# Kernel tuning notes

Hardware: AMD Instinct MI355X
Metric: run time of the kernel (lower is better)

Reference implementation:

```python
import jax, jax.numpy as jnp
import numpy as np

N = 150000   # total supergraph nodes (entities+events+chains)
D = 128      # embed_size
H = 4        # attention heads
DH = D // H  # head dim
E = 300000   # edges per layer
L = 4        # layer_specs length
A = 8        # edge attr dim
T = 10       # num_edge_type
TIME_SCALE = 24.0
SLOPE = 0.2  # negative_slope


def setup_inputs() -> dict:
    key = jax.random.key(0)
    ks = jax.random.split(key, 16)
    nrm = lambda k, s, sc=1.0: jax.random.normal(k, s, dtype=jnp.float32) * sc
    return {
        'x': nrm(ks[0], (N, D), 0.1),
        'Wq': nrm(ks[1], (L, D, D), D ** -0.5),
        'Wk': nrm(ks[2], (L, D, D), D ** -0.5),
        'Wv': nrm(ks[3], (L, D, D), D ** -0.5),
        'Wskip': nrm(ks[4], (L, D, D), D ** -0.5),
        'Wa': nrm(ks[5], (L, A, D), 0.1),
        'time_w': nrm(ks[6], (D,)),
        'time_b': nrm(ks[7], (D,), 0.1),
        'dist_w': nrm(ks[8], (D,)),
        'dist_b': nrm(ks[9], (D,), 0.1),
        'type_table': nrm(ks[10], (T, D), 0.1),
        'bn_gamma': jnp.ones((L, D), jnp.float32),
        'bn_beta': jnp.zeros((L, D), jnp.float32),
        'beta': jnp.full((L,), 0.5, jnp.float32),
        'edge_attr': jax.random.uniform(ks[11], (L, E, A), dtype=jnp.float32),
        'edge_dt': jax.random.uniform(ks[12], (L, E), dtype=jnp.float32) * TIME_SCALE,
        'edge_ds': jax.random.uniform(ks[13], (L, E), dtype=jnp.float32) * 10.0,
        'edge_index': jax.random.randint(ks[14], (L, 2, E), 0, N),
        'edge_type': jax.random.randint(ks[15], (L, E), 0, T),
    }


def _layer(x, Wq, Wk, Wv, Wskip, Wa, time_w, time_b, dist_w, dist_b,
           type_table, gamma, bvec, beta, attr, dt, ds, ei, et):
    n = x.shape[0]
    src, dst = ei[0], ei[1]
    # continuous time / distance encoders: cos basis (TimeEncoder / 'time' DistanceEncoder)
    te = jnp.cos((dt / TIME_SCALE)[:, None] * time_w + time_b)   # [E,D]
    de = jnp.cos(ds[:, None] * dist_w + dist_b)                  # [E,D]
    # 'add' edge/time fusion: attr MLP + time + dist + edge-type embeddings
    edge_feat = attr @ Wa + te + de + type_table[et]             # [E,D]
    kv_in = x[src] + edge_feat                                   # gather + fuse
    q = (x @ Wq).reshape(n, H, DH)[dst]                          # [E,H,DH]
    k = (kv_in @ Wk).reshape(-1, H, DH)
    v = (kv_in @ Wv).reshape(-1, H, DH)
    logits = (q * k).sum(-1) * (DH ** -0.5)                      # [E,H]
    logits = jnp.where(logits >= 0, logits, SLOPE * logits)      # leaky_relu(negative_slope)
    # segment softmax over incoming edges of each destination node
    m = jax.ops.segment_max(logits, dst, num_segments=n)
    a = jnp.exp(logits - m[dst])
    denom = jax.ops.segment_sum(a, dst, num_segments=n)
    a = a / denom[dst]
    agg = jax.ops.segment_sum(a[..., None] * v, dst, num_segments=n).reshape(n, D)
    # beta-weighted residual (learn_beta) with skip projection
    out = beta * (x @ Wskip) + (1.0 - beta) * agg
    # BatchNorm1d (training-mode batch stats) + ReLU
    mu = out.mean(0)
    var = out.var(0)
    out = (out - mu) * jax.lax.rsqrt(var + 1e-5) * gamma + bvec
    return jax.nn.relu(out)


def reference(x, Wq, Wk, Wv, Wskip, Wa, time_w, time_b, dist_w, dist_b,
              type_table, bn_gamma, bn_beta, beta, edge_attr, edge_dt,
              edge_ds, edge_index, edge_type):
    for l in range(L):  # entity2event, event2event, event2chain (time filter), chain2chain
        x = _layer(x, Wq[l], Wk[l], Wv[l], Wskip[l], Wa[l],
                   time_w, time_b, dist_w, dist_b, type_table,
                   bn_gamma[l], bn_beta[l], beta[l],
                   edge_attr[l], edge_dt[l], edge_ds[l],
                   edge_index[l], edge_type[l])
    return x
```

## Files before the change

kernel.cpp:

```cpp
#include <hip/hip_runtime.h>

typedef unsigned int u32;
typedef unsigned short u16;
typedef short bf16x8 __attribute__((ext_vector_type(8)));
typedef float f32x4 __attribute__((ext_vector_type(4)));

#define N_NODES 150000
#define E_EDGES 300000
#define L_CNT   151552
#define ETILES  9375
#define NTILES  4688

__device__ __forceinline__ float blo(u32 u){ return __uint_as_float(u << 16); }
__device__ __forceinline__ float bhi(u32 u){ return __uint_as_float(u & 0xffff0000u); }
__device__ __forceinline__ float b2f(u16 h){ return __uint_as_float(((u32)h) << 16); }
__device__ __forceinline__ u16 f2bf(float f){
  u32 u = __float_as_uint(f);
  return (u16)((u + 0x7fffu + ((u >> 16) & 1u)) >> 16);
}
__device__ __forceinline__ u32 pack2(float a, float b){
  return (u32)f2bf(a) | ((u32)f2bf(b) << 16);
}

__device__ __forceinline__ f32x4 mfma16(bf16x8 a, bf16x8 b, f32x4 c){
  return __builtin_amdgcn_mfma_f32_16x16x32_bf16(a, b, c, 0, 0, 0);
}

__device__ __forceinline__ int opsw(int r, int k){ return (r * 128 + k) ^ ((r & 7) << 3); }
__device__ __forceinline__ int csw(int r, int n){ return (r * 128 + n) ^ (((r >> 2) & 3) << 3); }

__global__ __launch_bounds__(256)
void k_wt(const float* __restrict__ Wq, const float* __restrict__ Wk,
          const float* __restrict__ Wv, const float* __restrict__ Ws,
          u16* __restrict__ Wt)
{
  const int m = blockIdx.x;
  const float* src = (m < 4 ? Wq : m < 8 ? Wk : m < 12 ? Wv : Ws)
                     + (size_t)(m & 3) * 16384;
  u16* dst = Wt + (size_t)m * 16384;
  const int t = threadIdx.x;
  for (int i = 0; i < 16; ++i) {
    int idx = i * 256 + t;
    int n = idx >> 5;
    int k4 = (idx & 31) << 2;
    ushort4 o;
    o.x = f2bf(src[(k4 + 0) * 128 + n]);
    o.y = f2bf(src[(k4 + 1) * 128 + n]);
    o.z = f2bf(src[(k4 + 2) * 128 + n]);
    o.w = f2bf(src[(k4 + 3) * 128 + n]);
    *(ushort4*)(dst + n * 128 + k4) = o;
  }
}


__global__ __launch_bounds__(256)
void k_hist(const int* __restrict__ eidx, int* __restrict__ counts)
{
  const int l = blockIdx.y;
  const int e = blockIdx.x * 256 + threadIdx.x;
  if (e < E_EDGES) {
    int dst = eidx[(size_t)l * 2 * E_EDGES + E_EDGES + e];
    atomicAdd(&counts[(size_t)l * L_CNT + dst], 1);
  }
}

__global__ __launch_bounds__(256)
void k_scan1(const int* __restrict__ counts, int* __restrict__ rowptr,
             int* __restrict__ bsum)
{
  __shared__ int sh[256];
  const int b = blockIdx.x, l = blockIdx.y;
  const int t = threadIdx.x;
  const int* c = counts + (size_t)l * L_CNT + b * 2048;
  int* rp = rowptr + (size_t)l * L_CNT + b * 2048;
  int v[8]; int s = 0;
  #pragma unroll
  for (int j = 0; j < 8; ++j) { v[j] = c[t * 8 + j]; s += v[j]; }
  sh[t] = s; __syncthreads();
  for (int off = 1; off < 256; off <<= 1) {
    int x = (t >= off) ? sh[t - off] : 0;
    __syncthreads();
    sh[t] += x;
    __syncthreads();
  }
  int excl = (t == 0) ? 0 : sh[t - 1];
  if (t == 255) bsum[l * 128 + b] = sh[255];
  int run = excl;
  #pragma unroll
  for (int j = 0; j < 8; ++j) { rp[t * 8 + j] = run; run += v[j]; }
}

__global__ __launch_bounds__(128)
void k_scan2(int* __restrict__ bsum)
{
  __shared__ int sh[128];
  const int l = blockIdx.x, t = threadIdx.x;
  int v = (t < 74) ? bsum[l * 128 + t] : 0;
  sh[t] = v; __syncthreads();
  for (int off = 1; off < 128; off <<= 1) {
    int x = (t >= off) ? sh[t - off] : 0;
    __syncthreads();
    sh[t] += x;
    __syncthreads();
  }
  int excl = (t == 0) ? 0 : sh[t - 1];
  if (t < 74) bsum[l * 128 + t] = excl;
}

__global__ __launch_bounds__(256)
void k_scan3(int* __restrict__ rowptr, int* __restrict__ tmp,
             const int* __restrict__ bsum)
{
  const int l = blockIdx.y;
  const int q = blockIdx.x * 256 + threadIdx.x;
  int v = rowptr[(size_t)l * L_CNT + q] + bsum[l * 128 + (q >> 11)];
  rowptr[(size_t)l * L_CNT + q] = v;
  tmp[(size_t)l * L_CNT + q] = v;
}

__global__ __launch_bounds__(256)
void k_scatter(const int* __restrict__ srcP, const int* __restrict__ dstP,
               const int* __restrict__ etP, const float* __restrict__ dtP,
               const float* __restrict__ dsP, const float* __restrict__ attrP,
               int* __restrict__ tmpL, u32* __restrict__ meta)
{
  const int e = blockIdx.x * 256 + threadIdx.x;
  if (e < E_EDGES) {
    int dst = dstP[e];
    int pos = atomicAdd(&tmpL[dst], 1);
    int src = srcP[e];
    int et  = etP[e];
    float dtn = dtP[e] * (1.0f / 24.0f);
    float dsv = dsP[e];
    float4 aA = *(const float4*)(attrP + (size_t)e * 8);
    float4 aB = *(const float4*)(attrP + (size_t)e * 8 + 4);
    uint4 r0, r1;
    r0.x = (u32)src;
    r0.y = (u32)dst | ((u32)et << 20);
    r0.z = __float_as_uint(dtn);
    r0.w = __float_as_uint(dsv);
    r1.x = pack2(aA.x, aA.y); r1.y = pack2(aA.z, aA.w);
    r1.z = pack2(aB.x, aB.y); r1.w = pack2(aB.z, aB.w);
    u32* mp = meta + (size_t)pos * 8;
    *(uint4*)mp = r0;
    *(uint4*)(mp + 4) = r1;
  }
}

__global__ __launch_bounds__(128)
void bn_stats(const float* __restrict__ colsum, const float* __restrict__ colsumsq,
              const float* __restrict__ gamma, const float* __restrict__ bvec,
              float* __restrict__ scsh)
{
  const int d = threadIdx.x;
  const float invN = 1.f / 150000.f;
  float mu = colsum[d] * invN;
  float var = colsumsq[d] * invN - mu * mu;
  float sc = gamma[d] * rsqrtf(var + 1e-5f);
  scsh[d] = sc;
  scsh[128 + d] = bvec[d] - mu * sc;
}

template<int XF32, int BN>
__global__ __launch_bounds__(256)
void k_kvin(const void* __restrict__ xg, const float* __restrict__ Wa,
            const float* __restrict__ tw, const float* __restrict__ tb,
            const float* __restrict__ dw, const float* __restrict__ db,
            const float* __restrict__ ttab, const u32* __restrict__ meta,
            const float* __restrict__ scsh, u16* __restrict__ kvV)
{
  const int idx = blockIdx.x * 256 + threadIdx.x;
  const int e = idx >> 4;
  const int c8 = (idx & 15) << 3;
  const u32* mp = meta + (size_t)e * 8;
  uint4 m0 = *(const uint4*)mp;
  uint4 m1 = *(const uint4*)(mp + 4);
  const int src = (int)m0.x;
  const int et = (int)(m0.y >> 20);
  const float dtn = __uint_as_float(m0.z);
  const float dss = __uint_as_float(m0.w);
  float aa[8] = { blo(m1.x), bhi(m1.x), blo(m1.y), bhi(m1.y),
                  blo(m1.z), bhi(m1.z), blo(m1.w), bhi(m1.w) };
  const float4 twA = *(const float4*)(tw + c8);
  const float4 twB = *(const float4*)(tw + c8 + 4);
  const float4 tbA = *(const float4*)(tb + c8);
  const float4 tbB = *(const float4*)(tb + c8 + 4);
  const float4 dwA = *(const float4*)(dw + c8);
  const float4 dwB = *(const float4*)(dw + c8 + 4);
  const float4 dbA = *(const float4*)(db + c8);
  const float4 dbB = *(const float4*)(db + c8 + 4);
  const float4 ttA = *(const float4*)(ttab + et * 128 + c8);
  const float4 ttB = *(const float4*)(ttab + et * 128 + c8 + 4);
  float f[8];
  f[0] = __cosf(fmaf(dtn, twA.x, tbA.x)) + __cosf(fmaf(dss, dwA.x, dbA.x)) + ttA.x;
  f[1] = __cosf(fmaf(dtn, twA.y, tbA.y)) + __cosf(fmaf(dss, dwA.y, dbA.y)) + ttA.y;
  f[2] = __cosf(fmaf(dtn, twA.z, tbA.z)) + __cosf(fmaf(dss, dwA.z, dbA.z)) + ttA.z;
  f[3] = __cosf(fmaf(dtn, twA.w, tbA.w)) + __cosf(fmaf(dss, dwA.w, dbA.w)) + ttA.w;
  f[4] = __cosf(fmaf(dtn, twB.x, tbB.x)) + __cosf(fmaf(dss, dwB.x, dbB.x)) + ttB.x;
  f[5] = __cosf(fmaf(dtn, twB.y, tbB.y)) + __cosf(fmaf(dss, dwB.y, dbB.y)) + ttB.y;
  f[6] = __cosf(fmaf(dtn, twB.z, tbB.z)) + __cosf(fmaf(dss, dwB.z, dbB.z)) + ttB.z;
  f[7] = __cosf(fmaf(dtn, twB.w, tbB.w)) + __cosf(fmaf(dss, dwB.w, dbB.w)) + ttB.w;
  #pragma unroll
  for (int a = 0; a < 8; ++a) {
    float4 wA = *(const float4*)(Wa + a * 128 + c8);
    float4 wB = *(const float4*)(Wa + a * 128 + c8 + 4);
    f[0] = fmaf(aa[a], wA.x, f[0]);
    f[1] = fmaf(aa[a], wA.y, f[1]);
    f[2] = fmaf(aa[a], wA.z, f[2]);
    f[3] = fmaf(aa[a], wA.w, f[3]);
    f[4] = fmaf(aa[a], wB.x, f[4]);
    f[5] = fmaf(aa[a], wB.y, f[5]);
    f[6] = fmaf(aa[a], wB.z, f[6]);
    f[7] = fmaf(aa[a], wB.w, f[7]);
  }
  float xv[8];
  if (XF32) {
    float4 xA = *(const float4*)((const float*)xg + (size_t)src * 128 + c8);
    float4 xB = *(const float4*)((const float*)xg + (size_t)src * 128 + c8 + 4);
    xv[0] = xA.x; xv[1] = xA.y; xv[2] = xA.z; xv[3] = xA.w;
    xv[4] = xB.x; xv[5] = xB.y; xv[6] = xB.z; xv[7] = xB.w;
  } else {
    uint4 xr = *(const uint4*)((const u16*)xg + (size_t)src * 128 + c8);
    xv[0] = blo(xr.x); xv[1] = bhi(xr.x); xv[2] = blo(xr.y); xv[3] = bhi(xr.y);
    xv[4] = blo(xr.z); xv[5] = bhi(xr.z); xv[6] = blo(xr.w); xv[7] = bhi(xr.w);
  }
  if (BN) {
    float4 scA = *(const float4*)(scsh + c8);
    float4 scB = *(const float4*)(scsh + c8 + 4);
    float4 shA = *(const float4*)(scsh + 128 + c8);
    float4 shB = *(const float4*)(scsh + 128 + c8 + 4);
    xv[0] = fmaxf(fmaf(xv[0], scA.x, shA.x), 0.f);
    xv[1] = fmaxf(fmaf(xv[1], scA.y, shA.y), 0.f);
    xv[2] = fmaxf(fmaf(xv[2], scA.z, shA.z), 0.f);
    xv[3] = fmaxf(fmaf(xv[3], scA.w, shA.w), 0.f);
    xv[4] = fmaxf(fmaf(xv[4], scB.x, shB.x), 0.f);
    xv[5] = fmaxf(fmaf(xv[5], scB.y, shB.y), 0.f);
    xv[6] = fmaxf(fmaf(xv[6], scB.z, shB.z), 0.f);
    xv[7] = fmaxf(fmaf(xv[7], scB.w, shB.w), 0.f);
  }
  uint4 o;
  o.x = pack2(xv[0] + f[0], xv[1] + f[1]);
  o.y = pack2(xv[2] + f[2], xv[3] + f[3]);
  o.z = pack2(xv[4] + f[4], xv[5] + f[5]);
  o.w = pack2(xv[6] + f[6], xv[7] + f[7]);
  *(uint4*)(kvV + (size_t)e * 128 + c8) = o;
}


template<int XF32, int BN>
__global__ __launch_bounds__(128, 2)
void gemm_qs(const void* __restrict__ xg, const u16* __restrict__ WtQ,
             const u16* __restrict__ WtS, const float* __restrict__ scsh,
             u16* __restrict__ Qo, u16* __restrict__ So)
{
  __shared__ __align__(16) u16 As[4160];
  __shared__ __align__(16) u16 Bs[4160];
  const int t = threadIdx.x;
  const int w = t >> 6, lane = t & 63;
  const int lr = lane & 15, hi = lane >> 4;
  const int row0 = blockIdx.x * 32;
  const int nr = min(32, N_NODES - row0);
  const u16* Wt = w ? WtS : WtQ;
  u16* C = w ? So : Qo;

  bf16x8 wt[8][4];
  #pragma unroll
  for (int nb = 0; nb < 8; ++nb)
    #pragma unroll
    for (int ks = 0; ks < 4; ++ks)
      wt[nb][ks] = *(const bf16x8*)(Wt + (nb * 16 + lr) * 128 + ks * 32 + hi * 8);

  #pragma unroll
  for (int i = 0; i < 4; ++i) {
    int idx = i * 128 + t;
    int r = idx >> 4, c8 = (idx & 15) << 3;
    if (r < nr) {
      if (XF32) {
        float4 vA = *(const float4*)((const float*)xg + (size_t)(row0 + r) * 128 + c8);
        float4 vB = *(const float4*)((const float*)xg + (size_t)(row0 + r) * 128 + c8 + 4);
        uint4 o;
        o.x = pack2(vA.x, vA.y); o.y = pack2(vA.z, vA.w);
        o.z = pack2(vB.x, vB.y); o.w = pack2(vB.z, vB.w);
        *(uint4*)(As + opsw(r, c8)) = o;
      } else {
        uint4 v = *(const uint4*)((const u16*)xg + (size_t)(row0 + r) * 128 + c8);
        if (BN) {
          float4 scA = *(const float4*)(scsh + c8);
          float4 scB = *(const float4*)(scsh + c8 + 4);
          float4 shA = *(const float4*)(scsh + 128 + c8);
          float4 shB = *(const float4*)(scsh + 128 + c8 + 4);
          float e0v = fmaxf(fmaf(blo(v.x), scA.x, shA.x), 0.f);
          float e1v = fmaxf(fmaf(bhi(v.x), scA.y, shA.y), 0.f);
          float e2v = fmaxf(fmaf(blo(v.y), scA.z, shA.z), 0.f);
          float e3v = fmaxf(fmaf(bhi(v.y), scA.w, shA.w), 0.f);
          float e4v = fmaxf(fmaf(blo(v.z), scB.x, shB.x), 0.f);
          float e5v = fmaxf(fmaf(bhi(v.z), scB.y, shB.y), 0.f);
          float e6v = fmaxf(fmaf(blo(v.w), scB.z, shB.z), 0.f);
          float e7v = fmaxf(fmaf(bhi(v.w), scB.w, shB.w), 0.f);
          v.x = pack2(e0v, e1v); v.y = pack2(e2v, e3v);
          v.z = pack2(e4v, e5v); v.w = pack2(e6v, e7v);
        }
        *(uint4*)(As + opsw(r, c8)) = v;
      }
    } else {
      *(uint4*)(As + opsw(r, c8)) = make_uint4(0, 0, 0, 0);
    }
  }
  __syncthreads();

  f32x4 acc[2][8];
  #pragma unroll
  for (int a = 0; a < 2; ++a)
    #pragma unroll
    for (int b = 0; b < 8; ++b) {
      acc[a][b][0] = 0.f; acc[a][b][1] = 0.f;
      acc[a][b][2] = 0.f; acc[a][b][3] = 0.f;
    }
  #pragma unroll
  for (int ks = 0; ks < 4; ++ks) {
    const int kb = ks * 32 + hi * 8;
    bf16x8 a0 = *(const bf16x8*)(As + opsw(lr, kb));
    bf16x8 a1 = *(const bf16x8*)(As + opsw(16 + lr, kb));
    #pragma unroll
    for (int nb = 0; nb < 8; ++nb) {
      acc[0][nb] = mfma16(a0, wt[nb][ks], acc[0][nb]);
      acc[1][nb] = mfma16(a1, wt[nb][ks], acc[1][nb]);
    }
  }
  __syncthreads();

  u16* Cs = w ? Bs : As;
  const int g4 = hi << 2;
  #pragma unroll
  for (int mt = 0; mt < 2; ++mt)
    #pragma unroll
    for (int nt = 0; nt < 8; ++nt)
      #pragma unroll
      for (int j = 0; j < 4; ++j)
        Cs[csw(mt * 16 + g4 + j, nt * 16 + lr)] = f2bf(acc[mt][nt][j]);
  #pragma unroll
  for (int i = 0; i < 8; ++i) {
    int idx = i * 64 + lane;
    int r = idx >> 4, n8 = (idx & 15) << 3;
    if (r < nr) {
      uint4 v = *(const uint4*)(Cs + csw(r, n8));
      *(uint4*)(C + (size_t)(row0 + r) * 128 + n8) = v;
    }
  }
}


__global__ __launch_bounds__(128, 2)
void edge_kv(const u16* __restrict__ WtK, const u16* __restrict__ WtV,
             const u32* __restrict__ meta, const u16* __restrict__ Qb,
             u16* __restrict__ kvV, float* __restrict__ logits)
{
  __shared__ __align__(16) u16 KVs[4160];
  __shared__ __align__(16) u16 Qs[4160];
  __shared__ int dstSh[32];
  const int t = threadIdx.x;
  const int w = t >> 6, lane = t & 63;
  const int lr = lane & 15, hi = lane >> 4;
  const int e0 = blockIdx.x * 32;
  const u16* Wt = w ? WtV : WtK;

  bf16x8 wt[8][4];
  #pragma unroll
  for (int nb = 0; nb < 8; ++nb)
    #pragma unroll
    for (int ks = 0; ks < 4; ++ks)
      wt[nb][ks] = *(const bf16x8*)(Wt + (nb * 16 + lr) * 128 + ks * 32 + hi * 8);

  if (w == 0) {
    #pragma unroll
    for (int i = 0; i < 8; ++i) {
      int idx = i * 64 + lane;
      int r = idx >> 4, c8 = (idx & 15) << 3;
      uint4 v = *(const uint4*)(kvV + (size_t)(e0 + r) * 128 + c8);
      *(uint4*)(KVs + opsw(r, c8)) = v;
    }
  } else {
    if (lane < 32)
      dstSh[lane] = (int)(meta[(size_t)(e0 + lane) * 8 + 1] & 0xFFFFFu);
    #pragma unroll
    for (int i = 0; i < 8; ++i) {
      int idx = i * 64 + lane;
      int r = idx >> 4, c8 = (idx & 15) << 3;
      int qrow = dstSh[r];
      uint4 qv = *(const uint4*)(Qb + (size_t)qrow * 128 + c8);
      *(uint4*)(Qs + opsw(r, c8)) = qv;
    }
  }
  __syncthreads();

  if (w == 0) {
    #pragma unroll
    for (int eb = 0; eb < 2; ++eb) {
      f32x4 kacc[8];
      #pragma unroll
      for (int b = 0; b < 8; ++b) {
        kacc[b][0] = 0.f; kacc[b][1] = 0.f; kacc[b][2] = 0.f; kacc[b][3] = 0.f;
      }
      #pragma unroll
      for (int ks = 0; ks < 4; ++ks) {
        bf16x8 ef = *(const bf16x8*)(KVs + opsw(eb * 16 + lr, ks * 32 + hi * 8));
        #pragma unroll
        for (int nb = 0; nb < 8; ++nb)
          kacc[nb] = mfma16(wt[nb][ks], ef, kacc[nb]);
      }
      const int el = eb * 16 + lr;
      float hs[4] = {0.f, 0.f, 0.f, 0.f};
      #pragma unroll
      for (int nb = 0; nb < 8; ++nb) {
        ushort4 q = *(const ushort4*)(Qs + opsw(el, nb * 16 + hi * 4));
        hs[nb >> 1] += b2f(q.x) * kacc[nb][0] + b2f(q.y) * kacc[nb][1]
                     + b2f(q.z) * kacc[nb][2] + b2f(q.w) * kacc[nb][3];
      }
      #pragma unroll
      for (int h = 0; h < 4; ++h) {
        hs[h] += __shfl_xor(hs[h], 16, 64);
        hs[h] += __shfl_xor(hs[h], 32, 64);
        hs[h] *= 0.17677669529663687f;
        hs[h] = (hs[h] >= 0.f) ? hs[h] : 0.2f * hs[h];
      }
      if (lane < 16)
        *(float4*)(logits + (size_t)(e0 + el) * 4) = make_float4(hs[0], hs[1], hs[2], hs[3]);
    }
    __syncthreads();
  } else {
    f32x4 vacc[2][8];
    #pragma unroll
    for (int a = 0; a < 2; ++a)
      #pragma unroll
      for (int b = 0; b < 8; ++b) {
        vacc[a][b][0] = 0.f; vacc[a][b][1] = 0.f;
        vacc[a][b][2] = 0.f; vacc[a][b][3] = 0.f;
      }
    #pragma unroll
    for (int ks = 0; ks < 4; ++ks) {
      const int kb = ks * 32 + hi * 8;
      bf16x8 a0 = *(const bf16x8*)(KVs + opsw(lr, kb));
      bf16x8 a1 = *(const bf16x8*)(KVs + opsw(16 + lr, kb));
      #pragma unroll
      for (int nb = 0; nb < 8; ++nb) {
        vacc[0][nb] = mfma16(a0, wt[nb][ks], vacc[0][nb]);
        vacc[1][nb] = mfma16(a1, wt[nb][ks], vacc[1][nb]);
      }
    }
    __syncthreads();
    const int g4 = hi << 2;
    #pragma unroll
    for (int mt = 0; mt < 2; ++mt)
      #pragma unroll
      for (int nt = 0; nt < 8; ++nt)
        #pragma unroll
        for (int j = 0; j < 4; ++j)
          Qs[csw(mt * 16 + g4 + j, nt * 16 + lr)] = f2bf(vacc[mt][nt][j]);
    #pragma unroll
    for (int i = 0; i < 8; ++i) {
      int idx = i * 64 + lane;
      int r = idx >> 4, n8 = (idx & 15) << 3;
      uint4 v = *(const uint4*)(Qs + csw(r, n8));
      *(uint4*)(kvV + (size_t)(e0 + r) * 128 + n8) = v;
    }
  }
}

template<int PREBF16>
__global__ __launch_bounds__(256)
void node_agg(const u16* __restrict__ Vs, const float* __restrict__ logits,
              const int* __restrict__ rowptr, const u16* __restrict__ S,
              const float* __restrict__ betaP, float* __restrict__ pre,
              u16* __restrict__ preb, float* __restrict__ colsum,
              float* __restrict__ colsumsq)
{
  __shared__ float red[1024];
  const int t = threadIdx.x;
  const int g = t >> 5;
  const int lane = t & 31;
  const int d0 = lane * 4;
  const int h = lane >> 3;
  const float beta = *betaP;
  const float omb = 1.f - beta;
  float s4[4] = {0.f, 0.f, 0.f, 0.f};
  float q4[4] = {0.f, 0.f, 0.f, 0.f};
  for (int rep = 0; rep < 16; ++rep) {
    int n = blockIdx.x * 128 + rep * 8 + g;
    if (n < N_NODES) {
      int rs = rowptr[n], re = rowptr[n + 1];
      float m = -1e30f;
      for (int i = rs; i < re; ++i)
        m = fmaxf(m, logits[(size_t)i * 4 + h]);
      float den = 0.f;
      float a0 = 0.f, a1 = 0.f, a2 = 0.f, a3 = 0.f;
      for (int i = rs; i < re; ++i) {
        float wgt = __expf(logits[(size_t)i * 4 + h] - m);
        den += wgt;
        ushort4 v = *(const ushort4*)(Vs + (size_t)i * 128 + d0);
        a0 = fmaf(wgt, b2f(v.x), a0);
        a1 = fmaf(wgt, b2f(v.y), a1);
        a2 = fmaf(wgt, b2f(v.z), a2);
        a3 = fmaf(wgt, b2f(v.w), a3);
      }
      float inv = (den > 0.f) ? (omb / den) : 0.f;
      ushort4 sv = *(const ushort4*)(S + (size_t)n * 128 + d0);
      float p0 = fmaf(beta, b2f(sv.x), a0 * inv);
      float p1 = fmaf(beta, b2f(sv.y), a1 * inv);
      float p2 = fmaf(beta, b2f(sv.z), a2 * inv);
      float p3 = fmaf(beta, b2f(sv.w), a3 * inv);
      if (PREBF16) {
        ushort4 o;
        o.x = f2bf(p0); o.y = f2bf(p1); o.z = f2bf(p2); o.w = f2bf(p3);
        *(ushort4*)(preb + (size_t)n * 128 + d0) = o;
      } else {
        *(float4*)(pre + (size_t)n * 128 + d0) = make_float4(p0, p1, p2, p3);
      }
      s4[0] += p0; s4[1] += p1; s4[2] += p2; s4[3] += p3;
      q4[0] += p0 * p0; q4[1] += p1 * p1; q4[2] += p2 * p2; q4[3] += p3 * p3;
    }
  }
  *(float4*)(&red[g * 128 + d0]) = make_float4(s4[0], s4[1], s4[2], s4[3]);
  __syncthreads();
  if (t < 128) {
    float tot = 0.f;
    #pragma unroll
    for (int gg = 0; gg < 8; ++gg) tot += red[gg * 128 + t];
    atomicAdd(&colsum[t], tot);
  }
  __syncthreads();
  *(float4*)(&red[g * 128 + d0]) = make_float4(q4[0], q4[1], q4[2], q4[3]);
  __syncthreads();
  if (t < 128) {
    float tot = 0.f;
    #pragma unroll
    for (int gg = 0; gg < 8; ++gg) tot += red[gg * 128 + t];
    atomicAdd(&colsumsq[t], tot);
  }
}

__global__ __launch_bounds__(256)
void bn_apply(const float* __restrict__ pre, const float* __restrict__ colsum,
              const float* __restrict__ colsumsq, const float* __restrict__ gamma,
              const float* __restrict__ bvec, float* __restrict__ outf)
{
  const int idx = blockIdx.x * 256 + threadIdx.x;
  const int n = idx >> 5;
  const int d0 = (idx & 31) * 4;
  const float invN = 1.f / 150000.f;
  float4 p = *(const float4*)(pre + (size_t)n * 128 + d0);
  float4 cs = *(const float4*)(colsum + d0);
  float4 cq = *(const float4*)(colsumsq + d0);
  float4 gm = *(const float4*)(gamma + d0);
  float4 bv = *(const float4*)(bvec + d0);
  float mu, var, y;
  mu = cs.x * invN; var = cq.x * invN - mu * mu;
  y = (p.x - mu) * rsqrtf(var + 1e-5f) * gm.x + bv.x; p.x = fmaxf(y, 0.f);
  mu = cs.y * invN; var = cq.y * invN - mu * mu;
  y = (p.y - mu) * rsqrtf(var + 1e-5f) * gm.y + bv.y; p.y = fmaxf(y, 0.f);
  mu = cs.z * invN; var = cq.z * invN - mu * mu;
  y = (p.z - mu) * rsqrtf(var + 1e-5f) * gm.z + bv.z; p.z = fmaxf(y, 0.f);
  mu = cs.w * invN; var = cq.w * invN - mu * mu;
  y = (p.w - mu) * rsqrtf(var + 1e-5f) * gm.w + bv.w; p.w = fmaxf(y, 0.f);
  *(float4*)(outf + (size_t)n * 128 + d0) = p;
}

extern "C" void kernel_launch(void* const* d_in, const int* in_sizes, int n_in,
                              void* d_out, int out_size, void* d_ws, size_t ws_size,
                              hipStream_t stream)
{
  const float* x0    = (const float*)d_in[0];
  const float* Wq    = (const float*)d_in[1];
  const float* Wk    = (const float*)d_in[2];
  const float* Wv    = (const float*)d_in[3];
  const float* Wsk   = (const float*)d_in[4];
  const float* Wa    = (const float*)d_in[5];
  const float* tw    = (const float*)d_in[6];
  const float* tb    = (const float*)d_in[7];
  const float* dw    = (const float*)d_in[8];
  const float* db    = (const float*)d_in[9];
  const float* ttab  = (const float*)d_in[10];
  const float* gam   = (const float*)d_in[11];
  const float* bet   = (const float*)d_in[12];
  const float* betaP = (const float*)d_in[13];
  const float* attr  = (const float*)d_in[14];
  const float* dt    = (const float*)d_in[15];
  const float* dsv   = (const float*)d_in[16];
  const int*   eidx  = (const int*)d_in[17];
  const int*   etyp  = (const int*)d_in[18];

  char* p = (char*)d_ws;
  u16* xbf  = (u16*)p;       p += 38400000;
  u16* Q    = (u16*)p;       p += 38400000;
  u16* S    = (u16*)p;       p += 38400000;
  u16* kvV  = (u16*)p;       p += 76800000;
  float* logits = (float*)p; p += 4800000;
  int* rowptr = (int*)p;     p += 4 * L_CNT * 4;
  int* tmp    = (int*)p;     p += 4 * L_CNT * 4;
  int* bsum   = (int*)p;     p += 4 * 128 * 4;
  float* colsum   = (float*)p; p += 512;
  float* colsumsq = (float*)p; p += 512;
  float* scsh     = (float*)p; p += 1024;
  u16* Wt = (u16*)p;         p += 16 * 16384 * 2;
  u32* meta = (u32*)p;       p += (size_t)E_EDGES * 32;

  float* pre = (float*)d_out;

  k_wt<<<16, 256, 0, stream>>>(Wq, Wk, Wv, Wsk, Wt);
  hipMemsetAsync(tmp, 0, 4 * L_CNT * 4, stream);
  k_hist<<<dim3(1172, 4), 256, 0, stream>>>(eidx, tmp);
  k_scan1<<<dim3(74, 4), 256, 0, stream>>>(tmp, rowptr, bsum);
  k_scan2<<<4, 128, 0, stream>>>(bsum);
  k_scan3<<<dim3(592, 4), 256, 0, stream>>>(rowptr, tmp, bsum);

  for (int l = 0; l < 4; ++l) {
    const int* srcA = eidx + (size_t)l * 600000;
    const int* dstA = srcA + 300000;
    const int* rpl = rowptr + (size_t)l * L_CNT;
    const u16* WtQl = Wt + (size_t)l * 16384;
    const u16* WtKl = Wt + (size_t)(4 + l) * 16384;
    const u16* WtVl = Wt + (size_t)(8 + l) * 16384;
    const u16* WtSl = Wt + (size_t)(12 + l) * 16384;
    const float* Wal = Wa + (size_t)l * 1024;

    k_scatter<<<1172, 256, 0, stream>>>(
        srcA, dstA, etyp + (size_t)l * 300000, dt + (size_t)l * 300000,
        dsv + (size_t)l * 300000, attr + (size_t)l * 2400000,
        tmp + (size_t)l * L_CNT, meta);

    hipMemsetAsync(colsum, 0, 1024, stream);

    if (l == 0) {
      k_kvin<1, 0><<<18750, 256, 0, stream>>>((const void*)x0, Wal, tw, tb, dw, db,
                                              ttab, meta, scsh, kvV);
      gemm_qs<1, 0><<<NTILES, 128, 0, stream>>>((const void*)x0, WtQl, WtSl, scsh, Q, S);
    } else {
      k_kvin<0, 1><<<18750, 256, 0, stream>>>((const void*)xbf, Wal, tw, tb, dw, db,
                                              ttab, meta, scsh, kvV);
      gemm_qs<0, 1><<<NTILES, 128, 0, stream>>>((const void*)xbf, WtQl, WtSl, scsh, Q, S);
    }

    edge_kv<<<ETILES, 128, 0, stream>>>(WtKl, WtVl, meta, Q, kvV, logits);

    if (l < 3) {
      node_agg<1><<<1172, 256, 0, stream>>>(kvV, logits, rpl, S, betaP + l,
                                            nullptr, xbf, colsum, colsumsq);
      bn_stats<<<1, 128, 0, stream>>>(colsum, colsumsq, gam + (size_t)l * 128,
                                      bet + (size_t)l * 128, scsh);
    } else {
      node_agg<0><<<1172, 256, 0, stream>>>(kvV, logits, rpl, S, betaP + l,
                                            pre, nullptr, colsum, colsumsq);
      bn_apply<<<18750, 256, 0, stream>>>(pre, colsum, colsumsq,
                                          gam + (size_t)l * 128,
                                          bet + (size_t)l * 128, (float*)d_out);
    }
  }
}
```

Before: 1.448 ms.

## Fuse edge-feature construction into edge_kv, removing separate k_kvin kernel

Drops the standalone k_kvin kernel that built the kv_in rows (cos time/distance encodings, attr projection, type embedding, gathered source features with BN+ReLU) and wrote them to global memory. edge_kv now computes these rows itself and writes them straight into shared memory before the K/V MFMAs. This removes one launch per layer plus a full E x 128 bf16 write and read-back. In exchange, edge_kv does extra ALU and gather work per block, which raises register pressure and may lower occupancy.

```diff
diff --git a/kernel.cpp b/kernel.cpp
--- a/kernel.cpp
+++ b/kernel.cpp
@@ -159,91 +159,6 @@
   float sc = gamma[d] * rsqrtf(var + 1e-5f);
   scsh[d] = sc;
   scsh[128 + d] = bvec[d] - mu * sc;
-}
-
-template<int XF32, int BN>
-__global__ __launch_bounds__(256)
-void k_kvin(const void* __restrict__ xg, const float* __restrict__ Wa,
-            const float* __restrict__ tw, const float* __restrict__ tb,
-            const float* __restrict__ dw, const float* __restrict__ db,
-            const float* __restrict__ ttab, const u32* __restrict__ meta,
-            const float* __restrict__ scsh, u16* __restrict__ kvV)
-{
-  const int idx = blockIdx.x * 256 + threadIdx.x;
-  const int e = idx >> 4;
-  const int c8 = (idx & 15) << 3;
-  const u32* mp = meta + (size_t)e * 8;
-  uint4 m0 = *(const uint4*)mp;
-  uint4 m1 = *(const uint4*)(mp + 4);
-  const int src = (int)m0.x;
-  const int et = (int)(m0.y >> 20);
-  const float dtn = __uint_as_float(m0.z);
-  const float dss = __uint_as_float(m0.w);
-  float aa[8] = { blo(m1.x), bhi(m1.x), blo(m1.y), bhi(m1.y),
-                  blo(m1.z), bhi(m1.z), blo(m1.w), bhi(m1.w) };
-  const float4 twA = *(const float4*)(tw + c8);
-  const float4 twB = *(const float4*)(tw + c8 + 4);
-  const float4 tbA = *(const float4*)(tb + c8);
-  const float4 tbB = *(const float4*)(tb + c8 + 4);
-  const float4 dwA = *(const float4*)(dw + c8);
-  const float4 dwB = *(const float4*)(dw + c8 + 4);
-  const float4 dbA = *(const float4*)(db + c8);
-  const float4 dbB = *(const float4*)(db + c8 + 4);
-  const float4 ttA = *(const float4*)(ttab + et * 128 + c8);
-  const float4 ttB = *(const float4*)(ttab + et * 128 + c8 + 4);
-  float f[8];
-  f[0] = __cosf(fmaf(dtn, twA.x, tbA.x)) + __cosf(fmaf(dss, dwA.x, dbA.x)) + ttA.x;
-  f[1] = __cosf(fmaf(dtn, twA.y, tbA.y)) + __cosf(fmaf(dss, dwA.y, dbA.y)) + ttA.y;
-  f[2] = __cosf(fmaf(dtn, twA.z, tbA.z)) + __cosf(fmaf(dss, dwA.z, dbA.z)) + ttA.z;
-  f[3] = __cosf(fmaf(dtn, twA.w, tbA.w)) + __cosf(fmaf(dss, dwA.w, dbA.w)) + ttA.w;
-  f[4] = __cosf(fmaf(dtn, twB.x, tbB.x)) + __cosf(fmaf(dss, dwB.x, dbB.x)) + ttB.x;
-  f[5] = __cosf(fmaf(dtn, twB.y, tbB.y)) + __cosf(fmaf(dss, dwB.y, dbB.y)) + ttB.y;
-  f[6] = __cosf(fmaf(dtn, twB.z, tbB.z)) + __cosf(fmaf(dss, dwB.z, dbB.z)) + ttB.z;
-  f[7] = __cosf(fmaf(dtn, twB.w, tbB.w)) + __cosf(fmaf(dss, dwB.w, dbB.w)) + ttB.w;
-  #pragma unroll
-  for (int a = 0; a < 8; ++a) {
-    float4 wA = *(const float4*)(Wa + a * 128 + c8);
-    float4 wB = *(const float4*)(Wa + a * 128 + c8 + 4);
-    f[0] = fmaf(aa[a], wA.x, f[0]);
-    f[1] = fmaf(aa[a], wA.y, f[1]);
-    f[2] = fmaf(aa[a], wA.z, f[2]);
-    f[3] = fmaf(aa[a], wA.w, f[3]);
-    f[4] = fmaf(aa[a], wB.x, f[4]);
-    f[5] = fmaf(aa[a], wB.y, f[5]);
-    f[6] = fmaf(aa[a], wB.z, f[6]);
-    f[7] = fmaf(aa[a], wB.w, f[7]);
-  }
-  float xv[8];
-  if (XF32) {
-    float4 xA = *(const float4*)((const float*)xg + (size_t)src * 128 + c8);
-    float4 xB = *(const float4*)((const float*)xg + (size_t)src * 128 + c8 + 4);
-    xv[0] = xA.x; xv[1] = xA.y; xv[2] = xA.z; xv[3] = xA.w;
-    xv[4] = xB.x; xv[5] = xB.y; xv[6] = xB.z; xv[7] = xB.w;
-  } else {
-    uint4 xr = *(const uint4*)((const u16*)xg + (size_t)src * 128 + c8);
-    xv[0] = blo(xr.x); xv[1] = bhi(xr.x); xv[2] = blo(xr.y); xv[3] = bhi(xr.y);
-    xv[4] = blo(xr.z); xv[5] = bhi(xr.z); xv[6] = blo(xr.w); xv[7] = bhi(xr.w);
-  }
-  if (BN) {
-    float4 scA = *(const float4*)(scsh + c8);
-    float4 scB = *(const float4*)(scsh + c8 + 4);
-    float4 shA = *(const float4*)(scsh + 128 + c8);
-    float4 shB = *(const float4*)(scsh + 128 + c8 + 4);
-    xv[0] = fmaxf(fmaf(xv[0], scA.x, shA.x), 0.f);
-    xv[1] = fmaxf(fmaf(xv[1], scA.y, shA.y), 0.f);
-    xv[2] = fmaxf(fmaf(xv[2], scA.z, shA.z), 0.f);
-    xv[3] = fmaxf(fmaf(xv[3], scA.w, shA.w), 0.f);
-    xv[4] = fmaxf(fmaf(xv[4], scB.x, shB.x), 0.f);
-    xv[5] = fmaxf(fmaf(xv[5], scB.y, shB.y), 0.f);
-    xv[6] = fmaxf(fmaf(xv[6], scB.z, shB.z), 0.f);
-    xv[7] = fmaxf(fmaf(xv[7], scB.w, shB.w), 0.f);
-  }
-  uint4 o;
-  o.x = pack2(xv[0] + f[0], xv[1] + f[1]);
-  o.y = pack2(xv[2] + f[2], xv[3] + f[3]);
-  o.z = pack2(xv[4] + f[4], xv[5] + f[5]);
-  o.w = pack2(xv[6] + f[6], xv[7] + f[7]);
-  *(uint4*)(kvV + (size_t)e * 128 + c8) = o;
 }
 
 
@@ -350,9 +265,14 @@
 }
 
 
+template<int XF32, int BN>
 __global__ __launch_bounds__(128, 2)
-void edge_kv(const u16* __restrict__ WtK, const u16* __restrict__ WtV,
-             const u32* __restrict__ meta, const u16* __restrict__ Qb,
+void edge_kv(const void* __restrict__ xg, const u16* __restrict__ WtK,
+             const u16* __restrict__ WtV, const float* __restrict__ Wa,
+             const float* __restrict__ tw, const float* __restrict__ tb,
+             const float* __restrict__ dw, const float* __restrict__ db,
+             const float* __restrict__ ttab, const u32* __restrict__ meta,
+             const u16* __restrict__ Qb, const float* __restrict__ scsh,
              u16* __restrict__ kvV, float* __restrict__ logits)
 {
   __shared__ __align__(16) u16 KVs[4160];
@@ -371,24 +291,94 @@
     for (int ks = 0; ks < 4; ++ks)
       wt[nb][ks] = *(const bf16x8*)(Wt + (nb * 16 + lr) * 128 + ks * 32 + hi * 8);
 
-  if (w == 0) {
+  const int c8 = (lane & 15) << 3;
+  #pragma unroll
+  for (int i = 0; i < 4; ++i) {
+    const int r = (w * 4 + i) * 4 + (lane >> 4);
+    const u32* mp = meta + (size_t)(e0 + r) * 8;
+    uint4 m0 = *(const uint4*)mp;
+    uint4 m1 = *(const uint4*)(mp + 4);
+    const int src = (int)m0.x;
+    const int et = (int)(m0.y >> 20);
+    const float dtn = __uint_as_float(m0.z);
+    const float dss = __uint_as_float(m0.w);
+    float4 twA = *(const float4*)(tw + c8);
+    float4 twB = *(const float4*)(tw + c8 + 4);
+    float4 tbA = *(const float4*)(tb + c8);
+    float4 tbB = *(const float4*)(tb + c8 + 4);
+    float4 dwA = *(const float4*)(dw + c8);
+    float4 dwB = *(const float4*)(dw + c8 + 4);
+    float4 dbA = *(const float4*)(db + c8);
+    float4 dbB = *(const float4*)(db + c8 + 4);
+    float4 ttA = *(const float4*)(ttab + et * 128 + c8);
+    float4 ttB = *(const float4*)(ttab + et * 128 + c8 + 4);
+    float f[8];
+    f[0] = __cosf(fmaf(dtn, twA.x, tbA.x)) + __cosf(fmaf(dss, dwA.x, dbA.x)) + ttA.x;
+    f[1] = __cosf(fmaf(dtn, twA.y, tbA.y)) + __cosf(fmaf(dss, dwA.y, dbA.y)) + ttA.y;
+    f[2] = __cosf(fmaf(dtn, twA.z, tbA.z)) + __cosf(fmaf(dss, dwA.z, dbA.z)) + ttA.z;
+    f[3] = __cosf(fmaf(dtn, twA.w, tbA.w)) + __cosf(fmaf(dss, dwA.w, dbA.w)) + ttA.w;
+    f[4] = __cosf(fmaf(dtn, twB.x, tbB.x)) + __cosf(fmaf(dss, dwB.x, dbB.x)) + ttB.x;
+    f[5] = __cosf(fmaf(dtn, twB.y, tbB.y)) + __cosf(fmaf(dss, dwB.y, dbB.y)) + ttB.y;
+    f[6] = __cosf(fmaf(dtn, twB.z, tbB.z)) + __cosf(fmaf(dss, dwB.z, dbB.z)) + ttB.z;
+    f[7] = __cosf(fmaf(dtn, twB.w, tbB.w)) + __cosf(fmaf(dss, dwB.w, dbB.w)) + ttB.w;
+    float aa[8] = { blo(m1.x), bhi(m1.x), blo(m1.y), bhi(m1.y),
+                    blo(m1.z), bhi(m1.z), blo(m1.w), bhi(m1.w) };
+    #pragma unroll
+    for (int a = 0; a < 8; ++a) {
+      float4 wA = *(const float4*)(Wa + a * 128 + c8);
+      float4 wB = *(const float4*)(Wa + a * 128 + c8 + 4);
+      f[0] = fmaf(aa[a], wA.x, f[0]);
+      f[1] = fmaf(aa[a], wA.y, f[1]);
+      f[2] = fmaf(aa[a], wA.z, f[2]);
+      f[3] = fmaf(aa[a], wA.w, f[3]);
+      f[4] = fmaf(aa[a], wB.x, f[4]);
+      f[5] = fmaf(aa[a], wB.y, f[5]);
+      f[6] = fmaf(aa[a], wB.z, f[6]);
+      f[7] = fmaf(aa[a], wB.w, f[7]);
+    }
+    float xv[8];
+    if (XF32) {
+      float4 xA = *(const float4*)((const float*)xg + (size_t)src * 128 + c8);
+      float4 xB = *(const float4*)((const float*)xg + (size_t)src * 128 + c8 + 4);
+      xv[0] = xA.x; xv[1] = xA.y; xv[2] = xA.z; xv[3] = xA.w;
+      xv[4] = xB.x; xv[5] = xB.y; xv[6] = xB.z; xv[7] = xB.w;
+    } else {
+      uint4 xr = *(const uint4*)((const u16*)xg + (size_t)src * 128 + c8);
+      xv[0] = blo(xr.x); xv[1] = bhi(xr.x); xv[2] = blo(xr.y); xv[3] = bhi(xr.y);
+      xv[4] = blo(xr.z); xv[5] = bhi(xr.z); xv[6] = blo(xr.w); xv[7] = bhi(xr.w);
+    }
+    if (BN) {
+      float4 scA = *(const float4*)(scsh + c8);
+      float4 scB = *(const float4*)(scsh + c8 + 4);
+      float4 shA = *(const float4*)(scsh + 128 + c8);
+      float4 shB = *(const float4*)(scsh + 128 + c8 + 4);
+      xv[0] = fmaxf(fmaf(xv[0], scA.x, shA.x), 0.f);
+      xv[1] = fmaxf(fmaf(xv[1], scA.y, shA.y), 0.f);
+      xv[2] = fmaxf(fmaf(xv[2], scA.z, shA.z), 0.f);
+      xv[3] = fmaxf(fmaf(xv[3], scA.w, shA.w), 0.f);
+      xv[4] = fmaxf(fmaf(xv[4], scB.x, shB.x), 0.f);
+      xv[5] = fmaxf(fmaf(xv[5], scB.y, shB.y), 0.f);
+      xv[6] = fmaxf(fmaf(xv[6], scB.z, shB.z), 0.f);
+      xv[7] = fmaxf(fmaf(xv[7], scB.w, shB.w), 0.f);
+    }
+    uint4 o;
+    o.x = pack2(xv[0] + f[0], xv[1] + f[1]);
+    o.y = pack2(xv[2] + f[2], xv[3] + f[3]);
+    o.z = pack2(xv[4] + f[4], xv[5] + f[5]);
+    o.w = pack2(xv[6] + f[6], xv[7] + f[7]);
+    *(uint4*)(KVs + opsw(r, c8)) = o;
+  }
+
+  if (w == 1) {
+    if (lane < 32)
+      dstSh[lane] = (int)(meta[(size_t)(e0 + lane) * 8 + 1] & 0xFFFFFu);
     #pragma unroll
     for (int i = 0; i < 8; ++i) {
       int idx = i * 64 + lane;
-      int r = idx >> 4, c8 = (idx & 15) << 3;
-      uint4 v = *(const uint4*)(kvV + (size_t)(e0 + r) * 128 + c8);
-      *(uint4*)(KVs + opsw(r, c8)) = v;
-    }
-  } else {
-    if (lane < 32)
-      dstSh[lane] = (int)(meta[(size_t)(e0 + lane) * 8 + 1] & 0xFFFFFu);
-    #pragma unroll
-    for (int i = 0; i < 8; ++i) {
-      int idx = i * 64 + lane;
-      int r = idx >> 4, c8 = (idx & 15) << 3;
+      int r = idx >> 4, cc8 = (idx & 15) << 3;
       int qrow = dstSh[r];
-      uint4 qv = *(const uint4*)(Qb + (size_t)qrow * 128 + c8);
-      *(uint4*)(Qs + opsw(r, c8)) = qv;
+      uint4 qv = *(const uint4*)(Qb + (size_t)qrow * 128 + cc8);
+      *(uint4*)(Qs + opsw(r, cc8)) = qv;
     }
   }
   __syncthreads();
@@ -630,16 +620,16 @@
     hipMemsetAsync(colsum, 0, 1024, stream);
 
     if (l == 0) {
-      k_kvin<1, 0><<<18750, 256, 0, stream>>>((const void*)x0, Wal, tw, tb, dw, db,
-                                              ttab, meta, scsh, kvV);
       gemm_qs<1, 0><<<NTILES, 128, 0, stream>>>((const void*)x0, WtQl, WtSl, scsh, Q, S);
+      edge_kv<1, 0><<<ETILES, 128, 0, stream>>>(
+          (const void*)x0, WtKl, WtVl, Wal, tw, tb, dw, db, ttab, meta, Q, scsh,
+          kvV, logits);
     } else {
-      k_kvin<0, 1><<<18750, 256, 0, stream>>>((const void*)xbf, Wal, tw, tb, dw, db,
-                                              ttab, meta, scsh, kvV);
       gemm_qs<0, 1><<<NTILES, 128, 0, stream>>>((const void*)xbf, WtQl, WtSl, scsh, Q, S);
-    }
-
-    edge_kv<<<ETILES, 128, 0, stream>>>(WtKl, WtVl, meta, Q, kvV, logits);
+      edge_kv<0, 1><<<ETILES, 128, 0, stream>>>(
+          (const void*)xbf, WtKl, WtVl, Wal, tw, tb, dw, db, ttab, meta, Q, scsh,
+          kvV, logits);
+    }
 
     if (l < 3) {
       node_agg<1><<<1172, 256, 0, stream>>>(kvV, logits, rpl, S, betaP + l,
```

After: 1.494 ms. +3.1%, slower.
